# Kernel optimization log

Measured on AMD Instinct MI355X. Metric: run time of the kernel, lower is better.

The kernel has to match this reference:

```python
import jax, jax.numpy as jnp
import numpy as np
from jax import lax


def setup_inputs() -> dict:
    key = jax.random.key(0)
    ks = jax.random.split(key, 8)
    B, T, F, H = 256, 96, 32, 1024
    s = 0.05
    return {
        "initial_input": jax.random.normal(ks[0], (B, 1, F), jnp.float32),
        "hidden_h": jax.random.normal(ks[1], (B, H), jnp.float32),
        "hidden_c": jax.random.normal(ks[2], (B, H), jnp.float32),
        "targets": jax.random.normal(ks[3], (B, T, F), jnp.float32),
        "W_x": jax.random.normal(ks[4], (F, 4 * H), jnp.float32) * s,
        "W_h": jax.random.normal(ks[5], (H, 4 * H), jnp.float32) * s,
        "b": jnp.zeros((4 * H,), jnp.float32),
        "W_dense": jax.random.normal(ks[6], (H, F), jnp.float32) * s,
        "b_dense": jnp.zeros((F,), jnp.float32),
    }


def reference(initial_input, hidden_h, hidden_c, targets, W_x, W_h, b, W_dense, b_dense):
    # Inference-mode (training=False) decode: no teacher forcing, each step's
    # dense output is fed back as the next LSTM input. Keras LSTM gate order: i, f, c(g), o.
    T = targets.shape[1]

    def step(carry, _):
        h, c, x = carry  # h,c: [B,H], x: [B,F]
        z = x @ W_x + h @ W_h + b            # [B, 4H]
        i, f, g, o = jnp.split(z, 4, axis=-1)
        i = jax.nn.sigmoid(i)
        f = jax.nn.sigmoid(f)
        g = jnp.tanh(g)
        o = jax.nn.sigmoid(o)
        c_new = f * c + i * g
        h_new = o * jnp.tanh(c_new)
        y = h_new @ W_dense + b_dense        # [B, F]
        return (h_new, c_new, y), y

    x0 = initial_input[:, 0, :]              # [B, F]
    _, ys = lax.scan(step, (hidden_h, hidden_c, x0), None, length=T)
    return jnp.transpose(ys, (1, 0, 2))      # [B, T, F]
```

## Files before the change

kernel.cpp:

```cpp
#include <hip/hip_runtime.h>
#include <hip/hip_bf16.h>
#include <stdint.h>

#define B_SZ 256
#define H_SZ 1024
#define NG   4096
#define F_SZ 32
#define T_SZ 96

typedef __attribute__((ext_vector_type(8))) short short8;
typedef __attribute__((ext_vector_type(4))) float f32x4;

__device__ __forceinline__ unsigned short f2bf(float x) {
  unsigned int u = __float_as_uint(x);
  u += 0x7fffu + ((u >> 16) & 1u);
  return (unsigned short)(u >> 16);
}
__device__ __forceinline__ float sigf(float x) {
  return 1.f / (1.f + __expf(-x));
}
__device__ __forceinline__ float tanh_fast(float x) {
  float e = __expf(-2.f * fabsf(x));
  float t = (1.f - e) / (1.f + e);
  return copysignf(t, x);
}
__device__ __forceinline__ void stage16(const void* g, void* l) {
  __builtin_amdgcn_global_load_lds(
      (const __attribute__((address_space(1))) void*)g,
      (__attribute__((address_space(3))) void*)l, 16, 0, 0);
}

__global__ __launch_bounds__(256) void k_prep_w(
    const float* __restrict__ Wx, const float* __restrict__ Wh,
    const float* __restrict__ Wd,
    unsigned short* __restrict__ WeffT, unsigned short* __restrict__ WhT,
    unsigned short* __restrict__ WdT, unsigned int* __restrict__ flags)
{
  int tid = threadIdx.x;
  if (blockIdx.x == 512) {
    for (int i = 0; i < 17; ++i) flags[i * 256 + tid] = 0u;
    for (int i = 0; i < 128; ++i) {
      int idx = i * 256 + tid;
      int f = idx >> 10, k = idx & 1023;
      WdT[idx] = f2bf(Wd[k * 32 + f]);
    }
    return;
  }
  __shared__ float wx[32 * 256];
  __shared__ unsigned short resE[32 * 256];
  __shared__ unsigned short resH[32 * 256];
  int kt = blockIdx.x & 31, nt = blockIdx.x >> 5;
  int k0 = kt * 32, n0 = nt * 256;
  for (int i = 0; i < 32; ++i) {
    int lin = i * 256 + tid;
    wx[lin] = Wx[(size_t)(lin >> 8) * NG + n0 + (lin & 255)];
  }
  __syncthreads();
  for (int kr = 0; kr < 32; ++kr) {
    int k = k0 + kr;
    float v = Wh[(size_t)k * NG + n0 + tid];
    float acc = 0.f;
#pragma unroll
    for (int f = 0; f < 32; ++f) acc += Wd[k * 32 + f] * wx[f * 256 + tid];
    resH[kr * 256 + tid] = f2bf(v);
    resE[kr * 256 + tid] = f2bf(v + acc);
  }
  __syncthreads();
#pragma unroll
  for (int pass = 0; pass < 2; ++pass) {
    const unsigned short* res = pass ? resH : resE;
    unsigned short* dst = (pass ? WhT : WeffT) + (size_t)(n0 + tid) * H_SZ + k0;
    unsigned int vals[16];
#pragma unroll
    for (int p = 0; p < 16; ++p)
      vals[p] = (unsigned int)res[(2 * p) * 256 + tid] |
                ((unsigned int)res[(2 * p + 1) * 256 + tid] << 16);
#pragma unroll
    for (int qd = 0; qd < 4; ++qd) {
      uint4 v4; v4.x = vals[4*qd]; v4.y = vals[4*qd+1]; v4.z = vals[4*qd+2]; v4.w = vals[4*qd+3];
      ((uint4*)dst)[qd] = v4;
    }
  }
}

__global__ __launch_bounds__(256, 1) void k_persist(
    const unsigned short* __restrict__ WeffT,
    const unsigned short* __restrict__ WhT,
    const float* __restrict__ x0,
    const float* __restrict__ h0,
    const float* __restrict__ c0,
    const float* __restrict__ Wx,
    const float* __restrict__ bvec,
    const float* __restrict__ bd,
    const unsigned short* __restrict__ WdT,
    unsigned short* __restrict__ hbuf0,
    unsigned short* __restrict__ hbuf1,
    float* __restrict__ out,
    unsigned int* __restrict__ flags)
{
  const int b = blockIdx.x;
  const int xcd = b & 7, slot = b >> 3;
  const int m0 = xcd << 5;
  const int nh = slot << 5;
  const int tid = threadIdx.x, lane = tid & 63, g = tid >> 6;

  __shared__ unsigned short Ab[32 * 1024];
  __shared__ float zlds[4][32][33];
  __shared__ float yp[8][32];
  __shared__ unsigned int sPure;

  unsigned int* xcctab = flags + 4096;
  unsigned int myxcc;
  asm volatile("s_getreg_b32 %0, hwreg(HW_REG_XCC_ID)" : "=s"(myxcc));
  myxcc &= 15u;

  float creg[4];
#pragma unroll
  for (int e = 0; e < 4; ++e) {
    int idx = e * 256 + tid;
    int m = idx >> 5, cc = idx & 31;
    size_t gi = (size_t)(m0 + m) * H_SZ + nh + cc;
    hbuf0[gi] = f2bf(h0[gi]);
    creg[e] = c0[gi];
  }
  __syncthreads();
  unsigned int* myflag = flags + (((xcd << 5) | slot) << 4);
  if (tid == 0) {
    __hip_atomic_store(&xcctab[b], myxcc, __ATOMIC_RELAXED,
                       __HIP_MEMORY_SCOPE_AGENT);
    __hip_atomic_store(myflag, 1u, __ATOMIC_RELEASE,
                       __HIP_MEMORY_SCOPE_AGENT);
  }

  const int col = lane & 15;
  const int kq = lane >> 4;
  const int n0a0 = (g << 10) + nh + col;
  const int n0a1 = n0a0 + 16;
  float bfv0 = bvec[n0a0], bfv1 = bvec[n0a1];
  float u0r[2][2][4];
#pragma unroll
  for (int mf = 0; mf < 2; ++mf)
#pragma unroll
    for (int e = 0; e < 4; ++e) { u0r[mf][0][e] = bfv0; u0r[mf][1][e] = bfv1; }
  for (int f = 0; f < 32; ++f) {
    float wx0 = Wx[(size_t)f * NG + n0a0];
    float wx1 = Wx[(size_t)f * NG + n0a1];
    bfv0 += bd[f] * wx0; bfv1 += bd[f] * wx1;
#pragma unroll
    for (int mf = 0; mf < 2; ++mf)
#pragma unroll
      for (int e = 0; e < 4; ++e) {
        float xv = x0[(m0 + mf * 16 + (kq << 2) + e) * 32 + f];
        u0r[mf][0][e] += xv * wx0;
        u0r[mf][1][e] += xv * wx1;
      }
  }

  short8 wr[2][32];
  {
    const unsigned short* p0 = WhT + (size_t)n0a0 * H_SZ + (kq << 3);
    const unsigned short* p1 = WhT + (size_t)n0a1 * H_SZ + (kq << 3);
#pragma unroll
    for (int kk = 0; kk < 32; ++kk) {
      wr[0][kk] = *(const short8*)(p0 + kk * 32);
      wr[1][kk] = *(const short8*)(p1 + kk * 32);
    }
  }

  const int srow = (tid & 127) >> 2;
  const int skg  = (tid & 3) ^ ((srow >> 1) & 3);
  const int sgbase = srow * H_SZ + ((tid >> 7) << 5) + (skg << 3);
  const int wdst = (tid >> 6) << 9;
  const int q = kq ^ ((col >> 1) & 3);
  const int aoff = col * 32 + (q << 3);
  const int yf = tid & 31, ykc = tid >> 5;
  const int ysw = (slot >> 1) & 3;
  const unsigned short* wdp = WdT + (size_t)yf * H_SZ + ykc * 128;

  bool pure = false;
  for (int j = 0; j <= T_SZ; ++j) {
    {
      const unsigned int tgt = (unsigned)(j + 1);
      if (g == 0 && lane < 32) {
        const unsigned int* fp = flags + (((xcd << 5) | lane) << 4);
        while (__hip_atomic_load(fp, __ATOMIC_RELAXED, __HIP_MEMORY_SCOPE_AGENT) < tgt)
          __builtin_amdgcn_s_sleep(1);
      }
      __syncthreads();
    }
    if (j == 0) {
      __builtin_amdgcn_fence(__ATOMIC_ACQUIRE, "agent");
      bool eq = true;
      if (g == 0 && lane < 32)
        eq = (__hip_atomic_load(&xcctab[(lane << 3) | xcd], __ATOMIC_RELAXED,
                                __HIP_MEMORY_SCOPE_AGENT) == myxcc);
      unsigned long long bal = __ballot(eq);
      if (tid == 0) sPure = (bal == ~0ull) ? 1u : 0u;
      __syncthreads();
      pure = (sPure != 0u);
    } else if (pure) {
      asm volatile("buffer_inv sc0" ::: "memory");
    } else {
      __builtin_amdgcn_fence(__ATOMIC_ACQUIRE, "agent");
    }
    const unsigned short* hp = (j & 1) ? hbuf1 : hbuf0;
    unsigned short* hn = (j & 1) ? hbuf0 : hbuf1;

    {
      const unsigned short* src = hp + (size_t)m0 * H_SZ + sgbase;
#pragma unroll
      for (int it = 0; it < 16; ++it)
        stage16(src + it * 64, &Ab[it * 2048 + wdst]);
      __syncthreads();
    }

    if (j >= 1) {
      float acc = 0.f;
#pragma unroll
      for (int c2 = 0; c2 < 4; ++c2)
#pragma unroll
        for (int p = 0; p < 4; ++p) {
          uint4 av = *(const uint4*)(Ab + (ykc * 4 + c2) * 1024 + slot * 32 + p * 8);
          uint4 wv = *(const uint4*)(wdp + c2 * 32 + ((p ^ ysw) << 3));
          acc += __uint_as_float(av.x << 16) * __uint_as_float(wv.x << 16);
          acc += __uint_as_float(av.x & 0xffff0000u) * __uint_as_float(wv.x & 0xffff0000u);
          acc += __uint_as_float(av.y << 16) * __uint_as_float(wv.y << 16);
          acc += __uint_as_float(av.y & 0xffff0000u) * __uint_as_float(wv.y & 0xffff0000u);
          acc += __uint_as_float(av.z << 16) * __uint_as_float(wv.z << 16);
          acc += __uint_as_float(av.z & 0xffff0000u) * __uint_as_float(wv.z & 0xffff0000u);
          acc += __uint_as_float(av.w << 16) * __uint_as_float(wv.w << 16);
          acc += __uint_as_float(av.w & 0xffff0000u) * __uint_as_float(wv.w & 0xffff0000u);
        }
      yp[ykc][yf] = acc;
    }

    if (j < T_SZ) {
      f32x4 acc[2][2];
#pragma unroll
      for (int mf = 0; mf < 2; ++mf)
#pragma unroll
        for (int e = 0; e < 4; ++e) {
          acc[mf][0][e] = (j == 0) ? u0r[mf][0][e] : bfv0;
          acc[mf][1][e] = (j == 0) ? u0r[mf][1][e] : bfv1;
        }
#pragma unroll
      for (int kk = 0; kk < 32; ++kk) {
        short8 a0 = *(const short8*)(Ab + kk * 1024 + aoff);
        short8 a1 = *(const short8*)(Ab + kk * 1024 + 512 + aoff);
        acc[0][0] = __builtin_amdgcn_mfma_f32_16x16x32_bf16(a0, wr[0][kk], acc[0][0], 0, 0, 0);
        acc[1][0] = __builtin_amdgcn_mfma_f32_16x16x32_bf16(a1, wr[0][kk], acc[1][0], 0, 0, 0);
        acc[0][1] = __builtin_amdgcn_mfma_f32_16x16x32_bf16(a0, wr[1][kk], acc[0][1], 0, 0, 0);
        acc[1][1] = __builtin_amdgcn_mfma_f32_16x16x32_bf16(a1, wr[1][kk], acc[1][1], 0, 0, 0);
      }
      if (j == 0) {
        const unsigned short* p0 = WeffT + (size_t)n0a0 * H_SZ + (kq << 3);
        const unsigned short* p1 = WeffT + (size_t)n0a1 * H_SZ + (kq << 3);
#pragma unroll
        for (int kk = 0; kk < 32; ++kk) {
          wr[0][kk] = *(const short8*)(p0 + kk * 32);
          wr[1][kk] = *(const short8*)(p1 + kk * 32);
        }
      }
#pragma unroll
      for (int mf = 0; mf < 2; ++mf)
#pragma unroll
        for (int nf = 0; nf < 2; ++nf)
#pragma unroll
          for (int e = 0; e < 4; ++e)
            zlds[g][mf * 16 + (kq << 2) + e][nf * 16 + col] = acc[mf][nf][e];
    }
    __syncthreads();

    if (j < T_SZ) {
#pragma unroll
      for (int e = 0; e < 4; ++e) {
        int idx = e * 256 + tid;
        int m = idx >> 5, cc = idx & 31;
        float zi = zlds[0][m][cc];
        float zf = zlds[1][m][cc];
        float zg = zlds[2][m][cc];
        float zo = zlds[3][m][cc];
        float iv = sigf(zi), fv = sigf(zf), gv = tanh_fast(zg), ov = sigf(zo);
        float cn = fv * creg[e] + iv * gv;
        creg[e] = cn;
        hn[(size_t)(m0 + m) * H_SZ + nh + cc] = f2bf(ov * tanh_fast(cn));
      }
    }
    if (j >= 1 && tid < 32) {
      float s = bd[tid];
#pragma unroll
      for (int kc = 0; kc < 8; ++kc) s += yp[kc][tid];
      out[(size_t)(m0 + slot) * (T_SZ * F_SZ) + (size_t)(j - 1) * F_SZ + tid] = s;
    }
    __syncthreads();
    if (tid == 0 && j < T_SZ) {
      if (pure)
        __hip_atomic_store(myflag, (unsigned)(j + 2), __ATOMIC_RELAXED,
                           __HIP_MEMORY_SCOPE_AGENT);
      else
        __hip_atomic_store(myflag, (unsigned)(j + 2), __ATOMIC_RELEASE,
                           __HIP_MEMORY_SCOPE_AGENT);
    }
  }
}

extern "C" void kernel_launch(void* const* d_in, const int* in_sizes, int n_in,
                              void* d_out, int out_size, void* d_ws, size_t ws_size,
                              hipStream_t stream)
{
  const float* x0 = (const float*)d_in[0];
  const float* h0 = (const float*)d_in[1];
  const float* c0 = (const float*)d_in[2];
  const float* Wx = (const float*)d_in[4];
  const float* Wh = (const float*)d_in[5];
  const float* bv = (const float*)d_in[6];
  const float* Wd = (const float*)d_in[7];
  const float* bd = (const float*)d_in[8];
  float* out = (float*)d_out;

  char* p = (char*)d_ws;
  unsigned short* WeffT = (unsigned short*)p; p += (size_t)NG * H_SZ * 2;
  unsigned short* WhT   = (unsigned short*)p; p += (size_t)NG * H_SZ * 2;
  unsigned short* WdT   = (unsigned short*)p; p += (size_t)F_SZ * H_SZ * 2;
  unsigned short* hb0   = (unsigned short*)p; p += (size_t)B_SZ * H_SZ * 2;
  unsigned short* hb1   = (unsigned short*)p; p += (size_t)B_SZ * H_SZ * 2;
  unsigned int* flags   = (unsigned int*)p;  p += 4352 * 4;
  (void)ws_size; (void)in_sizes; (void)n_in; (void)out_size;

  k_prep_w<<<dim3(513), dim3(256), 0, stream>>>(Wx, Wh, Wd, WeffT, WhT, WdT, flags);

  k_persist<<<dim3(256), dim3(256), 0, stream>>>(
      WeffT, WhT, x0, h0, c0, Wx, bv, bd, WdT, hb0, hb1, out, flags);
}
```

Baseline: 755.1 us.

## Split persistent LSTM block work across 8 waves instead of 4

Doubles the persistent kernel's block size to 512 threads. Each wave now owns one 16-column half of a gate tile, so it holds half the recurrent weight registers and issues half the MFMAs per step. The LDS staging, gate update, dense-output partial sums and reduction are all re-indexed for 8 waves, and the staging swizzle expression is rewritten to match. This aims to shorten the per-step serial critical path and add latency hiding. The cost is more threads contending for barriers and LDS, and possible register-pressure spills under the new launch bounds.

```diff
diff --git a/kernel.cpp b/kernel.cpp
--- a/kernel.cpp
+++ b/kernel.cpp
@@ -28,6 +28,9 @@
   __builtin_amdgcn_global_load_lds(
       (const __attribute__((address_space(1))) void*)g,
       (__attribute__((address_space(3))) void*)l, 16, 0, 0);
+}
+__device__ __forceinline__ short8 u4s8(uint4 v) {
+  union { uint4 u; short8 s; } c; c.u = v; return c.s;
 }
 
 __global__ __launch_bounds__(256) void k_prep_w(
@@ -83,7 +86,7 @@
   }
 }
 
-__global__ __launch_bounds__(256, 1) void k_persist(
+__global__ __launch_bounds__(512, 2) void k_persist(
     const unsigned short* __restrict__ WeffT,
     const unsigned short* __restrict__ WhT,
     const float* __restrict__ x0,
@@ -102,11 +105,13 @@
   const int xcd = b & 7, slot = b >> 3;
   const int m0 = xcd << 5;
   const int nh = slot << 5;
-  const int tid = threadIdx.x, lane = tid & 63, g = tid >> 6;
+  const int tid = threadIdx.x, lane = tid & 63, w = tid >> 6;
+  const int g = w >> 1;
+  const int nhh = (w & 1) << 4;
 
   __shared__ unsigned short Ab[32 * 1024];
   __shared__ float zlds[4][32][33];
-  __shared__ float yp[8][32];
+  __shared__ float yp[16][32];
   __shared__ unsigned int sPure;
 
   unsigned int* xcctab = flags + 4096;
@@ -114,10 +119,10 @@
   asm volatile("s_getreg_b32 %0, hwreg(HW_REG_XCC_ID)" : "=s"(myxcc));
   myxcc &= 15u;
 
-  float creg[4];
-#pragma unroll
-  for (int e = 0; e < 4; ++e) {
-    int idx = e * 256 + tid;
+  float creg[2];
+#pragma unroll
+  for (int e = 0; e < 2; ++e) {
+    int idx = e * 512 + tid;
     int m = idx >> 5, cc = idx & 31;
     size_t gi = (size_t)(m0 + m) * H_SZ + nh + cc;
     hbuf0[gi] = f2bf(h0[gi]);
@@ -134,54 +139,51 @@
 
   const int col = lane & 15;
   const int kq = lane >> 4;
-  const int n0a0 = (g << 10) + nh + col;
-  const int n0a1 = n0a0 + 16;
-  float bfv0 = bvec[n0a0], bfv1 = bvec[n0a1];
-  float u0r[2][2][4];
+  const int n0a = (g << 10) + nh + nhh + col;
+  float bfv = bvec[n0a];
+  float u0r[2][4];
 #pragma unroll
   for (int mf = 0; mf < 2; ++mf)
 #pragma unroll
-    for (int e = 0; e < 4; ++e) { u0r[mf][0][e] = bfv0; u0r[mf][1][e] = bfv1; }
+    for (int e = 0; e < 4; ++e) u0r[mf][e] = bfv;
   for (int f = 0; f < 32; ++f) {
-    float wx0 = Wx[(size_t)f * NG + n0a0];
-    float wx1 = Wx[(size_t)f * NG + n0a1];
-    bfv0 += bd[f] * wx0; bfv1 += bd[f] * wx1;
+    float wxf = Wx[(size_t)f * NG + n0a];
+    bfv += bd[f] * wxf;
 #pragma unroll
     for (int mf = 0; mf < 2; ++mf)
 #pragma unroll
       for (int e = 0; e < 4; ++e) {
         float xv = x0[(m0 + mf * 16 + (kq << 2) + e) * 32 + f];
-        u0r[mf][0][e] += xv * wx0;
-        u0r[mf][1][e] += xv * wx1;
-      }
-  }
-
-  short8 wr[2][32];
+        u0r[mf][e] += xv * wxf;
+      }
+  }
+
+  uint4 wr[32];
   {
-    const unsigned short* p0 = WhT + (size_t)n0a0 * H_SZ + (kq << 3);
-    const unsigned short* p1 = WhT + (size_t)n0a1 * H_SZ + (kq << 3);
-#pragma unroll
-    for (int kk = 0; kk < 32; ++kk) {
-      wr[0][kk] = *(const short8*)(p0 + kk * 32);
-      wr[1][kk] = *(const short8*)(p1 + kk * 32);
-    }
+    const unsigned short* p0 = WhT + (size_t)n0a * H_SZ + (kq << 3);
+#pragma unroll
+    for (int kk = 0; kk < 32; ++kk) wr[kk] = *(const uint4*)(p0 + kk * 32);
+#pragma unroll
+    for (int kk = 0; kk < 32; ++kk)
+      asm volatile("" : "+v"(wr[kk].x), "+v"(wr[kk].y),
+                        "+v"(wr[kk].z), "+v"(wr[kk].w));
   }
 
   const int srow = (tid & 127) >> 2;
-  const int skg  = (tid & 3) ^ ((srow >> 1) & 3);
+  const int skg  = (tid & 3) ^ ((tid >> 3) & 3);
   const int sgbase = srow * H_SZ + ((tid >> 7) << 5) + (skg << 3);
-  const int wdst = (tid >> 6) << 9;
+  const int wdst = w << 9;
   const int q = kq ^ ((col >> 1) & 3);
   const int aoff = col * 32 + (q << 3);
   const int yf = tid & 31, ykc = tid >> 5;
   const int ysw = (slot >> 1) & 3;
-  const unsigned short* wdp = WdT + (size_t)yf * H_SZ + ykc * 128;
+  const unsigned short* wdp = WdT + (size_t)yf * H_SZ + ykc * 64;
 
   bool pure = false;
   for (int j = 0; j <= T_SZ; ++j) {
     {
       const unsigned int tgt = (unsigned)(j + 1);
-      if (g == 0 && lane < 32) {
+      if (w == 0 && lane < 32) {
         const unsigned int* fp = flags + (((xcd << 5) | lane) << 4);
         while (__hip_atomic_load(fp, __ATOMIC_RELAXED, __HIP_MEMORY_SCOPE_AGENT) < tgt)
           __builtin_amdgcn_s_sleep(1);
@@ -191,7 +193,7 @@
     if (j == 0) {
       __builtin_amdgcn_fence(__ATOMIC_ACQUIRE, "agent");
       bool eq = true;
-      if (g == 0 && lane < 32)
+      if (w == 0 && lane < 32)
         eq = (__hip_atomic_load(&xcctab[(lane << 3) | xcd], __ATOMIC_RELAXED,
                                 __HIP_MEMORY_SCOPE_AGENT) == myxcc);
       unsigned long long bal = __ballot(eq);
@@ -209,18 +211,18 @@
     {
       const unsigned short* src = hp + (size_t)m0 * H_SZ + sgbase;
 #pragma unroll
-      for (int it = 0; it < 16; ++it)
-        stage16(src + it * 64, &Ab[it * 2048 + wdst]);
+      for (int it = 0; it < 8; ++it)
+        stage16(src + it * 128, &Ab[it * 4096 + wdst]);
       __syncthreads();
     }
 
     if (j >= 1) {
       float acc = 0.f;
 #pragma unroll
-      for (int c2 = 0; c2 < 4; ++c2)
+      for (int c2 = 0; c2 < 2; ++c2)
 #pragma unroll
         for (int p = 0; p < 4; ++p) {
-          uint4 av = *(const uint4*)(Ab + (ykc * 4 + c2) * 1024 + slot * 32 + p * 8);
+          uint4 av = *(const uint4*)(Ab + (ykc * 2 + c2) * 1024 + slot * 32 + p * 8);
           uint4 wv = *(const uint4*)(wdp + c2 * 32 + ((p ^ ysw) << 3));
           acc += __uint_as_float(av.x << 16) * __uint_as_float(wv.x << 16);
           acc += __uint_as_float(av.x & 0xffff0000u) * __uint_as_float(wv.x & 0xffff0000u);
@@ -235,46 +237,41 @@
     }
 
     if (j < T_SZ) {
-      f32x4 acc[2][2];
+      f32x4 acc2[2];
 #pragma unroll
       for (int mf = 0; mf < 2; ++mf)
 #pragma unroll
-        for (int e = 0; e < 4; ++e) {
-          acc[mf][0][e] = (j == 0) ? u0r[mf][0][e] : bfv0;
-          acc[mf][1][e] = (j == 0) ? u0r[mf][1][e] : bfv1;
-        }
+        for (int e = 0; e < 4; ++e)
+          acc2[mf][e] = (j == 0) ? u0r[mf][e] : bfv;
 #pragma unroll
       for (int kk = 0; kk < 32; ++kk) {
+        short8 bfr = u4s8(wr[kk]);
         short8 a0 = *(const short8*)(Ab + kk * 1024 + aoff);
         short8 a1 = *(const short8*)(Ab + kk * 1024 + 512 + aoff);
-        acc[0][0] = __builtin_amdgcn_mfma_f32_16x16x32_bf16(a0, wr[0][kk], acc[0][0], 0, 0, 0);
-        acc[1][0] = __builtin_amdgcn_mfma_f32_16x16x32_bf16(a1, wr[0][kk], acc[1][0], 0, 0, 0);
-        acc[0][1] = __builtin_amdgcn_mfma_f32_16x16x32_bf16(a0, wr[1][kk], acc[0][1], 0, 0, 0);
-        acc[1][1] = __builtin_amdgcn_mfma_f32_16x16x32_bf16(a1, wr[1][kk], acc[1][1], 0, 0, 0);
+        acc2[0] = __builtin_amdgcn_mfma_f32_16x16x32_bf16(a0, bfr, acc2[0], 0, 0, 0);
+        acc2[1] = __builtin_amdgcn_mfma_f32_16x16x32_bf16(a1, bfr, acc2[1], 0, 0, 0);
       }
       if (j == 0) {
-        const unsigned short* p0 = WeffT + (size_t)n0a0 * H_SZ + (kq << 3);
-        const unsigned short* p1 = WeffT + (size_t)n0a1 * H_SZ + (kq << 3);
-#pragma unroll
-        for (int kk = 0; kk < 32; ++kk) {
-          wr[0][kk] = *(const short8*)(p0 + kk * 32);
-          wr[1][kk] = *(const short8*)(p1 + kk * 32);
-        }
+        const unsigned short* p0 = WeffT + (size_t)n0a * H_SZ + (kq << 3);
+#pragma unroll
+        for (int kk = 0; kk < 32; ++kk) wr[kk] = *(const uint4*)(p0 + kk * 32);
+#pragma unroll
+        for (int kk = 0; kk < 32; ++kk)
+          asm volatile("" : "+v"(wr[kk].x), "+v"(wr[kk].y),
+                            "+v"(wr[kk].z), "+v"(wr[kk].w));
       }
 #pragma unroll
       for (int mf = 0; mf < 2; ++mf)
 #pragma unroll
-        for (int nf = 0; nf < 2; ++nf)
-#pragma unroll
-          for (int e = 0; e < 4; ++e)
-            zlds[g][mf * 16 + (kq << 2) + e][nf * 16 + col] = acc[mf][nf][e];
+        for (int e = 0; e < 4; ++e)
+          zlds[g][mf * 16 + (kq << 2) + e][nhh + col] = acc2[mf][e];
     }
     __syncthreads();
 
     if (j < T_SZ) {
 #pragma unroll
-      for (int e = 0; e < 4; ++e) {
-        int idx = e * 256 + tid;
+      for (int e = 0; e < 2; ++e) {
+        int idx = e * 512 + tid;
         int m = idx >> 5, cc = idx & 31;
         float zi = zlds[0][m][cc];
         float zf = zlds[1][m][cc];
@@ -289,7 +286,7 @@
     if (j >= 1 && tid < 32) {
       float s = bd[tid];
 #pragma unroll
-      for (int kc = 0; kc < 8; ++kc) s += yp[kc][tid];
+      for (int kc = 0; kc < 16; ++kc) s += yp[kc][tid];
       out[(size_t)(m0 + slot) * (T_SZ * F_SZ) + (size_t)(j - 1) * F_SZ + tid] = s;
     }
     __syncthreads();
@@ -329,6 +326,6 @@
 
   k_prep_w<<<dim3(513), dim3(256), 0, stream>>>(Wx, Wh, Wd, WeffT, WhT, WdT, flags);
 
-  k_persist<<<dim3(256), dim3(256), 0, stream>>>(
+  k_persist<<<dim3(256), dim3(512), 0, stream>>>(
       WeffT, WhT, x0, h0, c0, Wx, bv, bd, WdT, hb0, hb1, out, flags);
 }
```

After: 811.4 us. +7.5%, slower.
